# Performance work log

Measured on AMD Instinct MI355X. Metric: run time of the kernel, lower is better.

Reference implementation:

```python
import jax, jax.numpy as jnp
import numpy as np

TS = 1.5          # hard-coded sampling period in forward()
W_CENTER = 337.927  # hard-coded center frequency in forward()


def shg_mat(yta):
    """Vectorized createSHGmat: yta is a complex64 vector of length N.
    Row m: Ts * fftshift(fft(fftshift(yta * roll(yta, delay[m]) * shiftFactor))).
    torch.roll(x, s)[j] == x[(j - s) % N], matching the gather below."""
    N = yta.shape[0]
    delays_f = jnp.arange(-(N // 2), N // 2, dtype=jnp.float32)
    delays_i = jnp.arange(-(N // 2), N // 2, dtype=jnp.int32)
    shift_factor = jnp.exp(-1j * 2.0 * W_CENTER * TS * delays_f).astype(jnp.complex64)  # [N]
    idx = (jnp.arange(N, dtype=jnp.int32)[None, :] - delays_i[:, None]) % N  # [N, N]
    y_shift = yta[idx]                                    # [N(delay), N(elem)]
    prod = yta[None, :] * y_shift * shift_factor[None, :]  # elementwise, [N, N]
    prod = jnp.fft.fftshift(prod, axes=-1)
    mat = TS * jnp.fft.fftshift(jnp.fft.fft(prod, axis=-1), axes=-1)
    return mat  # complex64 [N, N]


def frog_error(Tref, Tmeas):
    """calcFrogError: scalar FROG error between reference and measured traces."""
    mu = jnp.sum(Tmeas @ Tref) / jnp.sum(Tref @ Tref)
    r = jnp.sum((Tmeas - mu * Tref) ** 2)
    norm = jnp.float32(Tmeas.size) * jnp.max(Tmeas) ** 2
    return jnp.sqrt(r / norm)


def setup_inputs() -> dict:
    key = jax.random.key(0)
    k1, k2, k3 = jax.random.split(key, 3)
    B, N = 8, 1024
    prediction = jax.random.normal(k1, (B, 2 * N), dtype=jnp.float32)
    label = jax.random.normal(k2, (B, 2 * N), dtype=jnp.float32)
    spectrogram = jax.random.uniform(k3, (N, N), dtype=jnp.float32)
    return {"prediction": prediction, "label": label, "spectrogram": spectrogram}


def reference(prediction, label, spectrogram):
    B, two_n = prediction.shape
    n = two_n // 2
    pred_analytical = (prediction[:, :n] + 1j * prediction[:, n:]).astype(jnp.complex64)  # [B, N]
    mats = jax.vmap(shg_mat)(pred_analytical)          # [B, N, N] complex64
    Tref = jnp.abs(mats)                               # predicted SHG trace magnitude
    errs = jax.vmap(lambda t: frog_error(t, spectrogram))(Tref)  # [B]
    # loss = (sum over batch of frog_error) / batch_size; masked MSE terms in the
    # original are computed but never added to the returned loss, so they are omitted.
    return jnp.mean(errs)
```

## Files before the change

### kernel.cpp

```cpp
#include <hip/hip_runtime.h>
#include <math.h>

#define N 1024
#define B_ 8
#define T_ 256
#define R_ 4
#define NREP 4
#define GX 129

#define OFF_SF      0
#define OFF_TW      2048
#define OFF_ROWSUM  10240
#define ZERO_START  18432
#define OFF_COLSUMM 18432
#define OFF_SUMM2   19456
#define OFF_MAXM    19457
#define OFF_SUMMT   19464
#define OFF_SUMTT   19472
#define OFF_COLT    20480
#define WS_END      (OFF_COLT + B_ * NREP * N)

#define S1(a) ((a) ^ (((a) >> 2) & 0x10))
#define S2(a) ((a) ^ (((a) >> 3) & 0x0C))
#define S3(a) ((a) ^ (((a) >> 5) & 0x07))
#define S4(a) ((a) ^ (((a) >> 5) & 0x07))

__device__ __forceinline__ float wave_sum(float v) {
    #pragma unroll
    for (int o = 32; o > 0; o >>= 1) v += __shfl_down(v, o, 64);
    return v;
}
__device__ __forceinline__ float wave_max(float v) {
    #pragma unroll
    for (int o = 32; o > 0; o >>= 1) v = fmaxf(v, __shfl_down(v, o, 64));
    return v;
}

__device__ __forceinline__ void load_tw(float tw[6], const float* __restrict__ p) {
    float4 v = *(const float4*)p;
    float2 w = *(const float2*)(p + 4);
    tw[0] = v.x; tw[1] = v.y; tw[2] = v.z; tw[3] = v.w; tw[4] = w.x; tw[5] = w.y;
}

__device__ __forceinline__ void bfly4(float xr[4], float xi[4], const float tw[6]) {
    float t0r = xr[0] + xr[2], t0i = xi[0] + xi[2];
    float t1r = xr[0] - xr[2], t1i = xi[0] - xi[2];
    float t2r = xr[1] + xr[3], t2i = xi[1] + xi[3];
    float t3r = xr[1] - xr[3], t3i = xi[1] - xi[3];
    float y1r = t1r + t3i, y1i = t1i - t3r;
    float y2r = t0r - t2r, y2i = t0i - t2i;
    float y3r = t1r - t3i, y3i = t1i + t3r;
    xr[0] = t0r + t2r;            xi[0] = t0i + t2i;
    xr[1] = y1r * tw[0] - y1i * tw[1]; xi[1] = y1r * tw[1] + y1i * tw[0];
    xr[2] = y2r * tw[2] - y2i * tw[3]; xi[2] = y2r * tw[3] + y2i * tw[2];
    xr[3] = y3r * tw[4] - y3i * tw[5]; xi[3] = y3r * tw[5] + y3i * tw[4];
}

__global__ __launch_bounds__(T_) void k_prep(float* ws, float* out) {
    const int e = blockIdx.x * T_ + threadIdx.x;
    {
        double ang = -2.0 * 337.927 * 1.5 * (double)(e - 512);
        double s, c;
        sincos(ang, &s, &c);
        ws[OFF_SF + 2 * e] = (float)c;
        ws[OFF_SF + 2 * e + 1] = (float)s;
    }
    {
        int s = e >> 8, tt = e & 255;
        int h = 256 >> (2 * s);
        int pos = tt & (h - 1);
        int step = 1 << (2 * s);
        double a1 = -2.0 * M_PI * (double)(pos * step) / 1024.0;
        double s1, c1, s2, c2, s3, c3;
        sincos(a1, &s1, &c1);
        sincos(2.0 * a1, &s2, &c2);
        sincos(3.0 * a1, &s3, &c3);
        float* p = ws + OFF_TW + e * 8;
        p[0] = (float)c1; p[1] = (float)s1;
        p[2] = (float)c2; p[3] = (float)s2;
        p[4] = (float)c3; p[5] = (float)s3;
        p[6] = 0.f; p[7] = 0.f;
    }
    for (int j = ZERO_START + e; j < WS_END; j += 4 * T_) ws[j] = 0.f;
    if (e == 0) out[0] = 0.f;
}

__global__ __launch_bounds__(T_, 6) void k_row(const float* __restrict__ pred,
                                               const float* __restrict__ M,
                                               float* __restrict__ ws) {
    __shared__ float Yr[N], Yi[N];
    __shared__ float Ar[N], Ai[N], Br[N], Bi[N];
    __shared__ float colA[N];
    __shared__ float red[R_ + 2][4];
    const int t = threadIdx.x;
    const int blk = blockIdx.x;
    const int b = blockIdx.y;
    const int wid = t >> 6, lane = t & 63;

    if (b == B_) {
        if (blk >= 64) return;
        const int r0 = blk * 16;
        float cs[4] = {0.f, 0.f, 0.f, 0.f};
        float sq = 0.f, mx = 0.f;
        for (int r = 0; r < 16; ++r) {
            const float* row = M + (size_t)(r0 + r) * N;
            #pragma unroll
            for (int q = 0; q < 4; ++q) {
                float v = row[t + T_ * q];
                cs[q] += v;
                sq += v * v;
                mx = fmaxf(mx, v);
            }
        }
        #pragma unroll
        for (int q = 0; q < 4; ++q) atomicAdd(&ws[OFF_COLSUMM + t + T_ * q], cs[q]);
        sq = wave_sum(sq);
        mx = wave_max(mx);
        if (lane == 0) { red[0][wid] = sq; red[1][wid] = mx; }
        __syncthreads();
        if (t == 0) {
            atomicAdd(&ws[OFF_SUMM2], red[0][0] + red[0][1] + red[0][2] + red[0][3]);
            float X = fmaxf(fmaxf(red[1][0], red[1][1]), fmaxf(red[1][2], red[1][3]));
            atomicMax((unsigned int*)ws + OFF_MAXM, __float_as_uint(X));
        }
        return;
    }

    const int nr = (blk == GX - 1) ? 1 : R_;
    const int m0 = blk * R_;

    {
        const float* pr = pred + (size_t)b * 2 * N;
        #pragma unroll
        for (int q = 0; q < 4; ++q) {
            int j = t + T_ * q;
            Yr[j] = pr[j];
            Yi[j] = pr[N + j];
            colA[j] = 0.f;
        }
    }

    float tw0[6], tw1[6], tw2[6], tw3[6];
    load_tw(tw0, ws + OFF_TW + (size_t)t * 8);
    load_tw(tw1, ws + OFF_TW + (size_t)(256 + t) * 8);
    load_tw(tw2, ws + OFF_TW + (size_t)(512 + t) * 8);
    load_tw(tw3, ws + OFF_TW + (size_t)(768 + t) * 8);
    __syncthreads();

    float mtacc = 0.f, ttacc = 0.f;
    float xr[4], xi[4];

    for (int r = 0; r < nr; ++r) {
        const int m = m0 + r;
        const int mm = (N - m) & (N - 1);
        const float w = (mm == m) ? 1.f : 2.f;

        {
            const float2* sf2 = (const float2*)(ws + OFF_SF);
            #pragma unroll
            for (int q = 0; q < 4; ++q) {
                int j = t + T_ * q;
                int s = (j - m + 512) & (N - 1);
                float ar = Yr[j], ai = Yi[j];
                float br = Yr[s], bi = Yi[s];
                float2 sv = sf2[j];
                float p_r = ar * br - ai * bi;
                float p_i = ar * bi + ai * br;
                xr[q] = p_r * sv.x - p_i * sv.y;
                xi[q] = p_r * sv.y + p_i * sv.x;
            }
            bfly4(xr, xi, tw0);
            #pragma unroll
            for (int q = 0; q < 4; ++q) { int a = t + 256 * q; Ar[a] = xr[q]; Ai[a] = xi[q]; }
        }
        __syncthreads();

        {
            int base = ((t >> 6) << 8) | (t & 63);
            #pragma unroll
            for (int q = 0; q < 4; ++q) { int a = base + (q << 6); xr[q] = Ar[a]; xi[q] = Ai[a]; }
            bfly4(xr, xi, tw1);
            #pragma unroll
            for (int q = 0; q < 4; ++q) { int a = S1(base + (q << 6)); Br[a] = xr[q]; Bi[a] = xi[q]; }
        }
        __syncthreads();

        {
            int base = ((t >> 4) << 6) | (t & 15);
            #pragma unroll
            for (int q = 0; q < 4; ++q) { int a = S1(base + (q << 4)); xr[q] = Br[a]; xi[q] = Bi[a]; }
            bfly4(xr, xi, tw2);
            #pragma unroll
            for (int q = 0; q < 4; ++q) { int a = S2(base + (q << 4)); Ar[a] = xr[q]; Ai[a] = xi[q]; }
        }
        __syncthreads();

        {
            int base = ((t >> 2) << 4) | (t & 3);
            #pragma unroll
            for (int q = 0; q < 4; ++q) { int a = S2(base + (q << 2)); xr[q] = Ar[a]; xi[q] = Ai[a]; }
            bfly4(xr, xi, tw3);
            #pragma unroll
            for (int q = 0; q < 4; ++q) { int a = S3(base + (q << 2)); Br[a] = xr[q]; Bi[a] = xi[q]; }
        }
        __syncthreads();

        {
            int base = t << 2;
            #pragma unroll
            for (int q = 0; q < 4; ++q) { int a = S3(base + q); xr[q] = Br[a]; xi[q] = Bi[a]; }
            float t0r = xr[0] + xr[2], t0i = xi[0] + xi[2];
            float t1r = xr[0] - xr[2], t1i = xi[0] - xi[2];
            float t2r = xr[1] + xr[3], t2i = xi[1] + xi[3];
            float t3r = xr[1] - xr[3], t3i = xi[1] - xi[3];
            float yr[4], yi[4];
            yr[0] = t0r + t2r; yi[0] = t0i + t2i;
            yr[1] = t1r + t3i; yi[1] = t1i - t3r;
            yr[2] = t0r - t2r; yi[2] = t0i - t2i;
            yr[3] = t1r - t3i; yi[3] = t1i + t3r;
            int r4t = ((t & 3) << 6) | (((t >> 2) & 3) << 4) | (((t >> 4) & 3) << 2) | ((t >> 6) & 3);
            #pragma unroll
            for (int q = 0; q < 4; ++q) {
                int c = ((q << 8) | r4t) ^ 512;
                Ar[S4(c)] = 1.5f * sqrtf(yr[q] * yr[q] + yi[q] * yi[q]);
            }
        }
        __syncthreads();

        {
            const float* Mrow = M + (size_t)m * N;
            const float* Mrow2 = M + (size_t)mm * N;
            float rs = 0.f;
            #pragma unroll
            for (int q = 0; q < 4; ++q) {
                int cc = t + 256 * q;
                float v = Ar[S4(cc)];
                rs += v;
                ttacc += w * v * v;
                float msum = Mrow[cc];
                if (mm != m) msum += Mrow2[cc];
                mtacc += msum * v;
                colA[cc] += w * v;
            }
            rs = wave_sum(rs);
            if (lane == 0) red[r][wid] = rs;
        }
        __syncthreads();
    }

    {
        float* colT = ws + OFF_COLT + (size_t)(b * NREP + (blk & (NREP - 1))) * N;
        #pragma unroll
        for (int q = 0; q < 4; ++q) {
            int cc = t + 256 * q;
            atomicAdd(&colT[cc], colA[cc]);
        }
        float mt = wave_sum(mtacc);
        float tt2 = wave_sum(ttacc);
        if (lane == 0) { red[R_][wid] = mt; red[R_ + 1][wid] = tt2; }
        __syncthreads();
        if (t == 0) {
            for (int r = 0; r < nr; ++r) {
                int m = m0 + r, mm = (N - m) & (N - 1);
                float R = red[r][0] + red[r][1] + red[r][2] + red[r][3];
                ws[OFF_ROWSUM + b * N + m] = R;
                if (mm != m) ws[OFF_ROWSUM + b * N + mm] = R;
            }
            atomicAdd(&ws[OFF_SUMMT + b], red[R_][0] + red[R_][1] + red[R_][2] + red[R_][3]);
            atomicAdd(&ws[OFF_SUMTT + b], red[R_ + 1][0] + red[R_ + 1][1] + red[R_ + 1][2] + red[R_ + 1][3]);
        }
    }
}

__global__ __launch_bounds__(T_) void k_final(float* ws, float* out) {
    __shared__ double redn[4], redd[4];
    const int b = blockIdx.x;
    const int t = threadIdx.x;
    const int wid = t >> 6, lane = t & 63;
    const float* rowsum = ws + OFF_ROWSUM + (size_t)b * N;
    double num = 0.0, den = 0.0;
    #pragma unroll
    for (int q = 0; q < 4; ++q) {
        int j = t + 256 * q;
        double r = (double)rowsum[j];
        float ct = 0.f;
        #pragma unroll
        for (int rep = 0; rep < NREP; ++rep)
            ct += ws[OFF_COLT + (size_t)(b * NREP + rep) * N + j];
        num += (double)ws[OFF_COLSUMM + j] * r;
        den += (double)ct * r;
    }
    #pragma unroll
    for (int o = 32; o > 0; o >>= 1) {
        num += __shfl_down(num, o, 64);
        den += __shfl_down(den, o, 64);
    }
    if (lane == 0) { redn[wid] = num; redd[wid] = den; }
    __syncthreads();
    if (t == 0) {
        double NUM = redn[0] + redn[1] + redn[2] + redn[3];
        double DEN = redd[0] + redd[1] + redd[2] + redd[3];
        double mu = NUM / DEN;
        double r = (double)ws[OFF_SUMM2] - 2.0 * mu * (double)ws[OFF_SUMMT + b]
                 + mu * mu * (double)ws[OFF_SUMTT + b];
        float mx = ws[OFF_MAXM];
        double norm = 1048576.0 * (double)mx * (double)mx;
        atomicAdd(out, (float)(sqrt(r / norm) / 8.0));
    }
}

extern "C" void kernel_launch(void* const* d_in, const int* in_sizes, int n_in,
                              void* d_out, int out_size, void* d_ws, size_t ws_size,
                              hipStream_t stream) {
    const float* pred = (const float*)d_in[0];
    const float* M = (const float*)d_in[2];
    float* ws = (float*)d_ws;
    float* out = (float*)d_out;

    k_prep<<<4, T_, 0, stream>>>(ws, out);
    dim3 grid(GX, B_ + 1);
    k_row<<<grid, T_, 0, stream>>>(pred, M, ws);
    k_final<<<B_, T_, 0, stream>>>(ws, out);
}
```

Baseline: 100.9 us.

## Halve rows per block, drop shared staging, keep per-row state in registers

Each block now processes 2 paired rows instead of 4, doubling the grid, and the launch bound is raised to 8 blocks per CU. The Yr/Yi and colA shared arrays are removed: input samples are read directly from global memory (cached), shift factors are held in registers, and column sums accumulate in registers. The second row ping-pongs between the A and B shared buffers to avoid a trailing barrier. The aim is lower LDS use and higher occupancy, at the cost of more global/cache reads of pred and more atomic traffic from twice as many blocks.

```diff
diff --git a/kernel.cpp b/kernel.cpp
--- a/kernel.cpp
+++ b/kernel.cpp
@@ -4,9 +4,9 @@
 #define N 1024
 #define B_ 8
 #define T_ 256
-#define R_ 4
+#define R_ 2
 #define NREP 4
-#define GX 129
+#define GX 257
 
 #define OFF_SF      0
 #define OFF_TW      2048
@@ -85,12 +85,111 @@
     if (e == 0) out[0] = 0.f;
 }
 
-__global__ __launch_bounds__(T_, 6) void k_row(const float* __restrict__ pred,
+__device__ __forceinline__ void fft_row(
+    int t, int m, float w,
+    const float* __restrict__ pr,
+    const float sfr[4], const float sfi[4],
+    const float tw0[6], const float tw1[6], const float tw2[6], const float tw3[6],
+    float* __restrict__ X0r, float* __restrict__ X0i,
+    float* __restrict__ X1r, float* __restrict__ X1i,
+    const float* __restrict__ M, int mm,
+    float colreg[4], float& mtacc, float& ttacc,
+    float red[][4], int rslot)
+{
+    float xr[4], xi[4];
+
+    #pragma unroll
+    for (int q = 0; q < 4; ++q) {
+        int j = t + T_ * q;
+        int s = (j - m + 512) & (N - 1);
+        float ar = pr[j], ai = pr[N + j];
+        float br = pr[s], bi = pr[N + s];
+        float p_r = ar * br - ai * bi;
+        float p_i = ar * bi + ai * br;
+        xr[q] = p_r * sfr[q] - p_i * sfi[q];
+        xi[q] = p_r * sfi[q] + p_i * sfr[q];
+    }
+    bfly4(xr, xi, tw0);
+    #pragma unroll
+    for (int q = 0; q < 4; ++q) { int a = t + 256 * q; X0r[a] = xr[q]; X0i[a] = xi[q]; }
+    __syncthreads();
+
+    {
+        int base = ((t >> 6) << 8) | (t & 63);
+        #pragma unroll
+        for (int q = 0; q < 4; ++q) { int a = base + (q << 6); xr[q] = X0r[a]; xi[q] = X0i[a]; }
+        bfly4(xr, xi, tw1);
+        #pragma unroll
+        for (int q = 0; q < 4; ++q) { int a = S1(base + (q << 6)); X1r[a] = xr[q]; X1i[a] = xi[q]; }
+    }
+    __syncthreads();
+
+    {
+        int base = ((t >> 4) << 6) | (t & 15);
+        #pragma unroll
+        for (int q = 0; q < 4; ++q) { int a = S1(base + (q << 4)); xr[q] = X1r[a]; xi[q] = X1i[a]; }
+        bfly4(xr, xi, tw2);
+        #pragma unroll
+        for (int q = 0; q < 4; ++q) { int a = S2(base + (q << 4)); X0r[a] = xr[q]; X0i[a] = xi[q]; }
+    }
+    __syncthreads();
+
+    {
+        int base = ((t >> 2) << 4) | (t & 3);
+        #pragma unroll
+        for (int q = 0; q < 4; ++q) { int a = S2(base + (q << 2)); xr[q] = X0r[a]; xi[q] = X0i[a]; }
+        bfly4(xr, xi, tw3);
+        #pragma unroll
+        for (int q = 0; q < 4; ++q) { int a = S3(base + (q << 2)); X1r[a] = xr[q]; X1i[a] = xi[q]; }
+    }
+    __syncthreads();
+
+    {
+        int base = t << 2;
+        #pragma unroll
+        for (int q = 0; q < 4; ++q) { int a = S3(base + q); xr[q] = X1r[a]; xi[q] = X1i[a]; }
+        float t0r = xr[0] + xr[2], t0i = xi[0] + xi[2];
+        float t1r = xr[0] - xr[2], t1i = xi[0] - xi[2];
+        float t2r = xr[1] + xr[3], t2i = xi[1] + xi[3];
+        float t3r = xr[1] - xr[3], t3i = xi[1] - xi[3];
+        float yr[4], yi[4];
+        yr[0] = t0r + t2r; yi[0] = t0i + t2i;
+        yr[1] = t1r + t3i; yi[1] = t1i - t3r;
+        yr[2] = t0r - t2r; yi[2] = t0i - t2i;
+        yr[3] = t1r - t3i; yi[3] = t1i + t3r;
+        int r4t = ((t & 3) << 6) | (((t >> 2) & 3) << 4) | (((t >> 4) & 3) << 2) | ((t >> 6) & 3);
+        #pragma unroll
+        for (int q = 0; q < 4; ++q) {
+            int c = ((q << 8) | r4t) ^ 512;
+            X0r[S4(c)] = 1.5f * sqrtf(yr[q] * yr[q] + yi[q] * yi[q]);
+        }
+    }
+    __syncthreads();
+
+    {
+        const float* Mrow = M + (size_t)m * N;
+        const float* Mrow2 = M + (size_t)mm * N;
+        float rs = 0.f;
+        #pragma unroll
+        for (int q = 0; q < 4; ++q) {
+            int cc = t + 256 * q;
+            float v = X0r[S4(cc)];
+            rs += v;
+            ttacc += w * v * v;
+            float msum = Mrow[cc];
+            if (mm != m) msum += Mrow2[cc];
+            mtacc += msum * v;
+            colreg[q] += w * v;
+        }
+        rs = wave_sum(rs);
+        if ((t & 63) == 0) red[rslot][t >> 6] = rs;
+    }
+}
+
+__global__ __launch_bounds__(T_, 8) void k_row(const float* __restrict__ pred,
                                                const float* __restrict__ M,
                                                float* __restrict__ ws) {
-    __shared__ float Yr[N], Yi[N];
     __shared__ float Ar[N], Ai[N], Br[N], Bi[N];
-    __shared__ float colA[N];
     __shared__ float red[R_ + 2][4];
     const int t = threadIdx.x;
     const int blk = blockIdx.x;
@@ -128,132 +227,45 @@
 
     const int nr = (blk == GX - 1) ? 1 : R_;
     const int m0 = blk * R_;
-
-    {
-        const float* pr = pred + (size_t)b * 2 * N;
+    const float* pr = pred + (size_t)b * 2 * N;
+
+    float sfr[4], sfi[4];
+    {
+        const float2* sf2 = (const float2*)(ws + OFF_SF);
         #pragma unroll
         for (int q = 0; q < 4; ++q) {
-            int j = t + T_ * q;
-            Yr[j] = pr[j];
-            Yi[j] = pr[N + j];
-            colA[j] = 0.f;
-        }
-    }
-
+            float2 sv = sf2[t + T_ * q];
+            sfr[q] = sv.x; sfi[q] = sv.y;
+        }
+    }
     float tw0[6], tw1[6], tw2[6], tw3[6];
     load_tw(tw0, ws + OFF_TW + (size_t)t * 8);
     load_tw(tw1, ws + OFF_TW + (size_t)(256 + t) * 8);
     load_tw(tw2, ws + OFF_TW + (size_t)(512 + t) * 8);
     load_tw(tw3, ws + OFF_TW + (size_t)(768 + t) * 8);
-    __syncthreads();
-
+
+    float colreg[4] = {0.f, 0.f, 0.f, 0.f};
     float mtacc = 0.f, ttacc = 0.f;
-    float xr[4], xi[4];
-
-    for (int r = 0; r < nr; ++r) {
-        const int m = m0 + r;
+
+    {
+        const int m = m0;
         const int mm = (N - m) & (N - 1);
         const float w = (mm == m) ? 1.f : 2.f;
-
-        {
-            const float2* sf2 = (const float2*)(ws + OFF_SF);
-            #pragma unroll
-            for (int q = 0; q < 4; ++q) {
-                int j = t + T_ * q;
-                int s = (j - m + 512) & (N - 1);
-                float ar = Yr[j], ai = Yi[j];
-                float br = Yr[s], bi = Yi[s];
-                float2 sv = sf2[j];
-                float p_r = ar * br - ai * bi;
-                float p_i = ar * bi + ai * br;
-                xr[q] = p_r * sv.x - p_i * sv.y;
-                xi[q] = p_r * sv.y + p_i * sv.x;
-            }
-            bfly4(xr, xi, tw0);
-            #pragma unroll
-            for (int q = 0; q < 4; ++q) { int a = t + 256 * q; Ar[a] = xr[q]; Ai[a] = xi[q]; }
-        }
-        __syncthreads();
-
-        {
-            int base = ((t >> 6) << 8) | (t & 63);
-            #pragma unroll
-            for (int q = 0; q < 4; ++q) { int a = base + (q << 6); xr[q] = Ar[a]; xi[q] = Ai[a]; }
-            bfly4(xr, xi, tw1);
-            #pragma unroll
-            for (int q = 0; q < 4; ++q) { int a = S1(base + (q << 6)); Br[a] = xr[q]; Bi[a] = xi[q]; }
-        }
-        __syncthreads();
-
-        {
-            int base = ((t >> 4) << 6) | (t & 15);
-            #pragma unroll
-            for (int q = 0; q < 4; ++q) { int a = S1(base + (q << 4)); xr[q] = Br[a]; xi[q] = Bi[a]; }
-            bfly4(xr, xi, tw2);
-            #pragma unroll
-            for (int q = 0; q < 4; ++q) { int a = S2(base + (q << 4)); Ar[a] = xr[q]; Ai[a] = xi[q]; }
-        }
-        __syncthreads();
-
-        {
-            int base = ((t >> 2) << 4) | (t & 3);
-            #pragma unroll
-            for (int q = 0; q < 4; ++q) { int a = S2(base + (q << 2)); xr[q] = Ar[a]; xi[q] = Ai[a]; }
-            bfly4(xr, xi, tw3);
-            #pragma unroll
-            for (int q = 0; q < 4; ++q) { int a = S3(base + (q << 2)); Br[a] = xr[q]; Bi[a] = xi[q]; }
-        }
-        __syncthreads();
-
-        {
-            int base = t << 2;
-            #pragma unroll
-            for (int q = 0; q < 4; ++q) { int a = S3(base + q); xr[q] = Br[a]; xi[q] = Bi[a]; }
-            float t0r = xr[0] + xr[2], t0i = xi[0] + xi[2];
-            float t1r = xr[0] - xr[2], t1i = xi[0] - xi[2];
-            float t2r = xr[1] + xr[3], t2i = xi[1] + xi[3];
-            float t3r = xr[1] - xr[3], t3i = xi[1] - xi[3];
-            float yr[4], yi[4];
-            yr[0] = t0r + t2r; yi[0] = t0i + t2i;
-            yr[1] = t1r + t3i; yi[1] = t1i - t3r;
-            yr[2] = t0r - t2r; yi[2] = t0i - t2i;
-            yr[3] = t1r - t3i; yi[3] = t1i + t3r;
-            int r4t = ((t & 3) << 6) | (((t >> 2) & 3) << 4) | (((t >> 4) & 3) << 2) | ((t >> 6) & 3);
-            #pragma unroll
-            for (int q = 0; q < 4; ++q) {
-                int c = ((q << 8) | r4t) ^ 512;
-                Ar[S4(c)] = 1.5f * sqrtf(yr[q] * yr[q] + yi[q] * yi[q]);
-            }
-        }
-        __syncthreads();
-
-        {
-            const float* Mrow = M + (size_t)m * N;
-            const float* Mrow2 = M + (size_t)mm * N;
-            float rs = 0.f;
-            #pragma unroll
-            for (int q = 0; q < 4; ++q) {
-                int cc = t + 256 * q;
-                float v = Ar[S4(cc)];
-                rs += v;
-                ttacc += w * v * v;
-                float msum = Mrow[cc];
-                if (mm != m) msum += Mrow2[cc];
-                mtacc += msum * v;
-                colA[cc] += w * v;
-            }
-            rs = wave_sum(rs);
-            if (lane == 0) red[r][wid] = rs;
-        }
-        __syncthreads();
+        fft_row(t, m, w, pr, sfr, sfi, tw0, tw1, tw2, tw3,
+                Ar, Ai, Br, Bi, M, mm, colreg, mtacc, ttacc, red, 0);
+    }
+    if (nr == R_) {
+        const int m = m0 + 1;
+        const int mm = (N - m) & (N - 1);
+        fft_row(t, m, 2.f, pr, sfr, sfi, tw0, tw1, tw2, tw3,
+                Br, Bi, Ar, Ai, M, mm, colreg, mtacc, ttacc, red, 1);
     }
 
     {
         float* colT = ws + OFF_COLT + (size_t)(b * NREP + (blk & (NREP - 1))) * N;
         #pragma unroll
         for (int q = 0; q < 4; ++q) {
-            int cc = t + 256 * q;
-            atomicAdd(&colT[cc], colA[cc]);
+            atomicAdd(&colT[t + 256 * q], colreg[q]);
         }
         float mt = wave_sum(mtacc);
         float tt2 = wave_sum(ttacc);
```

New measurement: 125.6 us. 24.5% more time.
